# Performance work log

Hardware: AMD Instinct MI355X
Metric: run time of the kernel (lower is better)

The kernel has to match this reference:

```python
import jax, jax.numpy as jnp
import numpy as np

B, S, E, H, D, L, V, O = 64, 512, 512, 8, 64, 4, 50000, 1000
KW, STRIDE = 5, 5
L_OUT = (S - KW) // STRIDE + 1  # 102


def setup_inputs() -> dict:
    key = jax.random.key(0)
    ks = jax.random.split(key, 20)
    sc = 0.02
    inp = {
        'tokens': jax.random.randint(ks[0], (B, S), 0, V, dtype=jnp.int32),
        'emb': jax.random.normal(ks[1], (V + 1, E), jnp.float32) * sc,
        'Wq': jax.random.normal(ks[2], (L, H, E, D), jnp.float32) * sc,
        'bq': jnp.zeros((L, H, D), jnp.float32),
        'Wk': jax.random.normal(ks[3], (L, H, E, D), jnp.float32) * sc,
        'bk': jnp.zeros((L, H, D), jnp.float32),
        'Wv': jax.random.normal(ks[4], (L, H, E, D), jnp.float32) * sc,
        'bv': jnp.zeros((L, H, D), jnp.float32),
        'Wo': jax.random.normal(ks[5], (L, H * D, E), jnp.float32) * sc,
        'bo': jnp.zeros((L, E), jnp.float32),
        'W1': jax.random.normal(ks[6], (L, E, 2 * E), jnp.float32) * sc,
        'b1': jnp.zeros((L, 2 * E), jnp.float32),
        'W2': jax.random.normal(ks[7], (L, 2 * E, E), jnp.float32) * sc,
        'b2': jnp.zeros((L, E), jnp.float32),
        'Wc': jax.random.normal(ks[8], (KW, E, 1), jnp.float32) * sc,
        'bc': jnp.zeros((1,), jnp.float32),
        'Wd': jax.random.normal(ks[9], (L_OUT, O), jnp.float32) * sc,
        'bd': jnp.zeros((O,), jnp.float32),
    }
    return inp


def _l2_normalize(x, eps=1e-12):
    # tf.math.l2_normalize: x / sqrt(max(sum(x^2), eps))
    sq = jnp.sum(x * x, axis=-1, keepdims=True)
    return x * jax.lax.rsqrt(jnp.maximum(sq, eps))


def _forward(tokens, emb, Wq, bq, Wk, bk, Wv, bv, Wo, bo, W1, b1, W2, b2, Wc, bc, Wd, bd):
    mask = jnp.sign(tokens).astype(jnp.float32)[..., None]  # [B,S,1]
    out = emb[tokens] * mask                                 # [B,S,E]
    scale = 1.0 / jnp.sqrt(jnp.float32(E))                   # note: scaled by EMBEDDING_DIM, as in source
    for i in range(L):
        # per-head QKV projections, batched over heads
        q = jnp.einsum('bse,hed->bhsd', out, Wq[i]) + bq[i][None, :, None, :]
        k = jnp.einsum('bse,hed->bhsd', out, Wk[i]) + bk[i][None, :, None, :]
        v = jnp.einsum('bse,hed->bhsd', out, Wv[i]) + bv[i][None, :, None, :]
        scores = jnp.einsum('bhsd,bhtd->bhst', q, k) * scale
        attn = jax.nn.softmax(scores, axis=-1)
        heads = jnp.einsum('bhst,bhtd->bhsd', attn, v)       # [B,H,S,D]
        cat = heads.transpose(0, 2, 1, 3).reshape(B, S, H * D)
        mh = cat @ Wo[i] + bo[i]
        out = _l2_normalize(out + mh)
        ff = jax.nn.relu(out @ W1[i] + b1[i]) @ W2[i] + b2[i]
        out = ff + out
    # Conv1D(1, 5, strides=5) then squeeze channel, Dense over seq-length axis, softmax
    conv = jax.lax.conv_general_dilated(
        out, Wc, window_strides=(STRIDE,), padding='VALID',
        dimension_numbers=('NWC', 'WIO', 'NWC')) + bc          # [B,L_OUT,1]
    pooled = jnp.squeeze(conv, axis=-1)                        # [B,L_OUT]
    logits = pooled @ Wd + bd                                  # [B,O]
    return jax.nn.softmax(logits, axis=-1)


def reference(tokens, emb, Wq, bq, Wk, bk, Wv, bv, Wo, bo, W1, b1, W2, b2, Wc, bc, Wd, bd):
    return _forward(tokens, emb, Wq, bq, Wk, bk, Wv, bv, Wo, bo, W1, b1, W2, b2, Wc, bc, Wd, bd)
```

## Files before the change

### kernel.cpp

```cpp
#include <hip/hip_runtime.h>
#include <cstddef>

constexpr int B_ = 64, S_ = 512, E_ = 512, H_ = 8, D_ = 64, L_ = 4, O_ = 1000;
constexpr int BS_ = B_ * S_;
constexpr int HD_ = H_ * D_;
constexpr int QS_ = 1536;
constexpr int LOUT_ = 102;
constexpr float SCALE_ = 0.04419417382415922f;

typedef __bf16 bf16x8 __attribute__((ext_vector_type(8)));
typedef __bf16 bf16x4 __attribute__((ext_vector_type(4)));
typedef __bf16 bf16x2 __attribute__((ext_vector_type(2)));
typedef float floatx4 __attribute__((ext_vector_type(4)));

__device__ inline void load16_lds(const __bf16* g, __bf16* l) {
  __builtin_amdgcn_global_load_lds(
      (const __attribute__((address_space(1))) void*)g,
      (__attribute__((address_space(3))) void*)l, 16, 0, 0);
}

__global__ __launch_bounds__(256) void transpose_bf16(
    const float* __restrict__ in, __bf16* __restrict__ out,
    int R, int C, int IZ, int OZL, int OZH) {
  __shared__ float t[32][33];
  int z = blockIdx.z;
  const float* inz = in + (size_t)z * IZ;
  __bf16* outz = out + (size_t)(z >> 3) * OZL + (size_t)(z & 7) * OZH;
  int c0 = blockIdx.x * 32, r0 = blockIdx.y * 32;
  int x = threadIdx.x, y = threadIdx.y;
#pragma unroll
  for (int j = 0; j < 32; j += 8) t[y + j][x] = inz[(size_t)(r0 + y + j) * C + c0 + x];
  __syncthreads();
#pragma unroll
  for (int j = 0; j < 32; j += 8)
    outz[(size_t)(c0 + y + j) * R + r0 + x] = (__bf16)t[x][y + j];
}

__global__ __launch_bounds__(256) void bias_concat(
    const float* __restrict__ bq, const float* __restrict__ bk,
    const float* __restrict__ bv, float* __restrict__ qkvb) {
  int idx = blockIdx.x * 256 + threadIdx.x;
  int l = idx / QS_, j = idx % QS_;
  float v;
  if (j < 512) v = bq[l * 512 + j];
  else if (j < 1024) v = bk[l * 512 + j - 512];
  else v = bv[l * 512 + j - 1024];
  qkvb[idx] = v;
}

__global__ __launch_bounds__(256) void embed_kernel(
    const int* __restrict__ tokens, const float* __restrict__ emb,
    float* __restrict__ X, __bf16* __restrict__ Ab) {
  int idx = blockIdx.x * 256 + threadIdx.x;
  int bs = idx >> 7;
  int e = (idx & 127) << 2;
  int tok = tokens[bs];
  float4 v;
  if (tok == 0) v = make_float4(0.f, 0.f, 0.f, 0.f);
  else v = *(const float4*)(emb + (size_t)tok * E_ + e);
  size_t off = (size_t)bs * E_ + e;
  *(float4*)(X + off) = v;
  bf16x4 b;
  b[0] = (__bf16)v.x; b[1] = (__bf16)v.y; b[2] = (__bf16)v.z; b[3] = (__bf16)v.w;
  *(bf16x4*)(Ab + off) = b;
}

#define GFENCE asm volatile("" ::: "memory")
#define GBAR  do { GFENCE; __builtin_amdgcn_s_barrier(); GFENCE; } while (0)

template <int RELU, int RES, int OUTF, int OUTB, int SCQ, int KT>
__global__ __launch_bounds__(512, 2) void gemm_bf16(
    const __bf16* __restrict__ A, const __bf16* __restrict__ Bt,
    const float* __restrict__ bias, const float* __restrict__ Rsd,
    float* __restrict__ Cf, __bf16* __restrict__ Cb, int N, int lda, int Nt) {
  __shared__ __align__(16) __bf16 smem[32768];
  int tid = threadIdx.x;
  int lane = tid & 63, w8 = tid >> 6;
  int wm = w8 & 1, wn = w8 >> 1;
  int q4 = lane >> 4, a_ = lane & 15;
  int Mt8 = (int)(gridDim.x / Nt) >> 3;
  int xcd = blockIdx.x & 7;
  int j = blockIdx.x >> 3;
  int rr = j % (2 * Nt), chunk = j / (2 * Nt);
  int mt = xcd * Mt8 + chunk * 2 + (rr & 1);
  int nt = rr >> 1;
  int m0 = mt * 256, n0 = nt * 256;
  const int ldb = KT * 32;
  int ci0 = tid, ci1 = 512 + tid;
  int r0s = ci0 >> 2, q0s = (ci0 & 3) ^ ((r0s >> 1) & 3);
  int r1s = ci1 >> 2, q1s = (ci1 & 3) ^ ((r1s >> 1) & 3);
  const __bf16* Ag = A + (size_t)m0 * lda;
  const __bf16* Bg = Bt + (size_t)n0 * ldb;

  floatx4 acc[8][4];
#pragma unroll
  for (int i = 0; i < 8; ++i)
#pragma unroll
    for (int jj = 0; jj < 4; ++jj) acc[i][jj] = (floatx4)(0.0f);

  auto STAGE = [&](int t, int s) {
    __bf16* Ad = smem + s * 8192;
    __bf16* Bd = smem + 16384 + s * 8192;
    int k0 = t * 32;
    load16_lds(Ag + (size_t)r0s * lda + k0 + q0s * 8, Ad + ci0 * 8);
    load16_lds(Ag + (size_t)r1s * lda + k0 + q1s * 8, Ad + ci1 * 8);
    load16_lds(Bg + (size_t)r0s * ldb + k0 + q0s * 8, Bd + ci0 * 8);
    load16_lds(Bg + (size_t)r1s * ldb + k0 + q1s * 8, Bd + ci1 * 8);
  };

  STAGE(0, 0);
  for (int t = 0; t < KT; ++t) {
    if (t + 1 < KT) {
      STAGE(t + 1, (t + 1) & 1);
      asm volatile("s_waitcnt vmcnt(4)" ::: "memory");
    } else {
      asm volatile("s_waitcnt vmcnt(0)" ::: "memory");
    }
    GBAR;
    const __bf16* As = smem + (t & 1) * 8192;
    const __bf16* Bs = smem + 16384 + (t & 1) * 8192;
    bf16x8 bfr[4];
#pragma unroll
    for (int nf = 0; nf < 4; ++nf) {
      int r_ = wn * 64 + nf * 16 + a_;
      bfr[nf] = *(const bf16x8*)&Bs[(r_ * 4 + (q4 ^ ((r_ >> 1) & 3))) * 8];
    }
#pragma unroll
    for (int mf = 0; mf < 8; ++mf) {
      int r_ = wm * 128 + mf * 16 + a_;
      bf16x8 af = *(const bf16x8*)&As[(r_ * 4 + (q4 ^ ((r_ >> 1) & 3))) * 8];
#pragma unroll
      for (int nf = 0; nf < 4; ++nf)
        acc[mf][nf] = __builtin_amdgcn_mfma_f32_16x16x32_bf16(bfr[nf], af,
                                                              acc[mf][nf], 0, 0, 0);
    }
    GBAR;
  }

#pragma unroll 1
  for (int pass = 0; pass < 2; ++pass) {
    GBAR;
    if (wm == pass) {
#pragma unroll
      for (int mf = 0; mf < 8; ++mf) {
        int lr = mf * 16 + a_;
        int m = m0 + pass * 128 + lr;
#pragma unroll
        for (int nf = 0; nf < 4; ++nf) {
          int nl = wn * 64 + nf * 16 + q4 * 4;
          int n = n0 + nl;
          float4 bi = *(const float4*)(bias + n);
          floatx4 v = acc[mf][nf];
          v[0] += bi.x; v[1] += bi.y; v[2] += bi.z; v[3] += bi.w;
          if (SCQ) { if (n < 512) v *= SCALE_; }
          if (RES) {
            float4 rv = *(const float4*)(Rsd + (size_t)m * N + n);
            v[0] += rv.x; v[1] += rv.y; v[2] += rv.z; v[3] += rv.w;
          }
          if (RELU) {
#pragma unroll
            for (int r = 0; r < 4; ++r) v[r] = fmaxf(v[r], 0.f);
          }
          if (OUTF) {
            float4 o = make_float4(v[0], v[1], v[2], v[3]);
            *(float4*)(Cf + (size_t)m * N + n) = o;
          }
          if (OUTB) {
            bf16x4 ob;
#pragma unroll
            for (int r = 0; r < 4; ++r) ob[r] = (__bf16)v[r];
            int ch = nl >> 3;
            *(bf16x4*)&smem[lr * 256 + (ch ^ (lr & 7)) * 8 + (q4 & 1) * 4] = ob;
          }
        }
      }
    }
    GBAR;
    if (OUTB) {
#pragma unroll
      for (int it = 0; it < 8; ++it) {
        int cid = it * 512 + tid;
        int row = cid >> 5, ch = cid & 31;
        bf16x8 val = *(const bf16x8*)&smem[row * 256 + (ch ^ (row & 7)) * 8];
        *(bf16x8*)(Cb + (size_t)(m0 + pass * 128 + row) * N + n0 + ch * 8) = val;
      }
    }
  }
}

__global__ __launch_bounds__(256, 2) void attn_bf16(__bf16* __restrict__ QKV) {
  __shared__ __align__(16) __bf16 Qs[256 * 64];
  __shared__ __align__(16) __bf16 Ks[64 * 64];
  __shared__ __align__(16) __bf16 Vt[64 * 64];
  __shared__ __align__(16) __bf16 Ps[64 * 64];
  int tid = threadIdx.x, lane = tid & 63, w = tid >> 6;
  int q4 = lane >> 4, a_ = lane & 15;
  int bid = blockIdx.x;
  int xg = bid & 7, slot = bid >> 3;
  int b = (slot >> 4) * 8 + xg;
  int r_ = slot & 15;
  int h = r_ >> 1;
  int s0 = (r_ & 1) * 256;
  size_t rowbase = (size_t)b * S_ * QS_ + h * 64;
  __bf16* Qg = QKV + rowbase;
  const __bf16* Kg = QKV + rowbase + 512;
  const __bf16* Vg = QKV + rowbase + 1024;
#pragma unroll
  for (int j = 0; j < 8; ++j) {
    int ci = j * 256 + w * 64 + lane;
    int row = ci >> 3, c = ci & 7, q = c ^ (row & 7);
    load16_lds(Qg + (size_t)(s0 + row) * QS_ + q * 8, Qs + (j * 256 + w * 64) * 8);
  }
  float mrow[4], lrow[4];
  floatx4 accO[4][4];
#pragma unroll
  for (int cc = 0; cc < 4; ++cc) {
    mrow[cc] = -3.0e38f; lrow[cc] = 0.f;
#pragma unroll
    for (int jc = 0; jc < 4; ++jc) accO[cc][jc] = (floatx4)(0.0f);
  }

  for (int t0 = 0; t0 < S_; t0 += 64) {
#pragma unroll
    for (int j = 0; j < 2; ++j) {
      int ci = j * 256 + w * 64 + lane;
      int row = ci >> 3, c = ci & 7, q = c ^ (row & 7);
      load16_lds(Kg + (size_t)(t0 + row) * QS_ + q * 8, Ks + (j * 256 + w * 64) * 8);
    }
    {
      int tp = tid & 31, dg = tid >> 5;
      bf16x8 v0 = *(const bf16x8*)(Vg + (size_t)(t0 + 2 * tp) * QS_ + dg * 8);
      bf16x8 v1 = *(const bf16x8*)(Vg + (size_t)(t0 + 2 * tp + 1) * QS_ + dg * 8);
#pragma unroll
      for (int x = 0; x < 8; ++x) {
        int d = dg * 8 + x;
        bf16x2 p; p[0] = v0[x]; p[1] = v1[x];
        *(bf16x2*)&Vt[(d * 8 + ((tp >> 2) ^ (d & 7))) * 8 + (tp & 3) * 2] = p;
      }
    }
    __syncthreads();
    bf16x8 af[2][4], bv[2][4];
#pragma unroll
    for (int ks = 0; ks < 2; ++ks)
#pragma unroll
      for (int jc = 0; jc < 4; ++jc) {
        int row = jc * 16 + a_, q = ks * 4 + q4;
        af[ks][jc] = *(const bf16x8*)&Ks[(row * 8 + (q ^ (row & 7))) * 8];
        bv[ks][jc] = *(const bf16x8*)&Vt[(row * 8 + (q ^ (row & 7))) * 8];
      }
#pragma unroll
    for (int cc = 0; cc < 4; ++cc) {
      int sbase = (cc * 4 + w) * 16;
      floatx4 sc[4];
#pragma unroll
      for (int jc = 0; jc < 4; ++jc) sc[jc] = (floatx4)(0.0f);
#pragma unroll
      for (int ks = 0; ks < 2; ++ks) {
        int row = sbase + a_, q = ks * 4 + q4;
        bf16x8 bq = *(const bf16x8*)&Qs[(row * 8 + (q ^ (row & 7))) * 8];
#pragma unroll
        for (int jc = 0; jc < 4; ++jc)
          sc[jc] = __builtin_amdgcn_mfma_f32_16x16x32_bf16(af[ks][jc], bq,
                                                           sc[jc], 0, 0, 0);
      }
      float mx = sc[0][0];
#pragma unroll
      for (int jc = 0; jc < 4; ++jc)
#pragma unroll
        for (int r = 0; r < 4; ++r) mx = fmaxf(mx, sc[jc][r]);
      mx = fmaxf(mx, __shfl_xor(mx, 16));
      mx = fmaxf(mx, __shfl_xor(mx, 32));
      float mnew = fmaxf(mrow[cc], mx);
      float alpha = __expf(mrow[cc] - mnew);
      mrow[cc] = mnew;
      float ps = 0.f;
      int prow = w * 16 + a_;
#pragma unroll
      for (int jc = 0; jc < 4; ++jc) {
        bf16x4 pb;
#pragma unroll
        for (int r = 0; r < 4; ++r) {
          float p = __expf(sc[jc][r] - mnew);
          ps += p;
          pb[r] = (__bf16)p;
        }
        int pc = jc * 2 + (q4 >> 1);
        *(bf16x4*)&Ps[(prow * 8 + (pc ^ (prow & 7))) * 8 + (q4 & 1) * 4] = pb;
      }
      ps += __shfl_xor(ps, 16);
      ps += __shfl_xor(ps, 32);
      lrow[cc] = lrow[cc] * alpha + ps;
      float aal[4];
#pragma unroll
      for (int r = 0; r < 4; ++r) aal[r] = __shfl(alpha, q4 * 4 + r);
#pragma unroll
      for (int jc = 0; jc < 4; ++jc) {
        floatx4 t = accO[cc][jc];
#pragma unroll
        for (int r = 0; r < 4; ++r) t[r] *= aal[r];
        accO[cc][jc] = t;
      }
#pragma unroll
      for (int ks = 0; ks < 2; ++ks) {
        int q = ks * 4 + q4;
        bf16x8 ap = *(const bf16x8*)&Ps[(prow * 8 + (q ^ (prow & 7))) * 8];
#pragma unroll
        for (int jc = 0; jc < 4; ++jc)
          accO[cc][jc] = __builtin_amdgcn_mfma_f32_16x16x32_bf16(
              ap, bv[ks][jc], accO[cc][jc], 0, 0, 0);
      }
    }
    __syncthreads();
  }
#pragma unroll
  for (int cc = 0; cc < 4; ++cc) {
    float inv = 1.f / lrow[cc];
    float linv[4];
#pragma unroll
    for (int r = 0; r < 4; ++r) linv[r] = __shfl(inv, q4 * 4 + r);
    int srow = s0 + (cc * 4 + w) * 16 + q4 * 4;
#pragma unroll
    for (int r = 0; r < 4; ++r)
#pragma unroll
      for (int jc = 0; jc < 4; ++jc)
        Qg[(size_t)(srow + r) * QS_ + jc * 16 + a_] =
            (__bf16)(accO[cc][jc][r] * linv[r]);
  }
}

__global__ __launch_bounds__(256) void addnorm_kernel(
    float* __restrict__ X, const __bf16* __restrict__ MH, __bf16* __restrict__ Ab) {
  int row = blockIdx.x * 4 + (threadIdx.x >> 6);
  int ln = threadIdx.x & 63;
  size_t off = (size_t)row * E_ + ln * 8;
  float xv[8];
  *(float4*)&xv[0] = *(const float4*)(X + off);
  *(float4*)&xv[4] = *(const float4*)(X + off + 4);
  bf16x8 mh = *(const bf16x8*)(MH + off);
  float ss = 0.f;
#pragma unroll
  for (int j = 0; j < 8; ++j) {
    xv[j] += (float)mh[j];
    ss += xv[j] * xv[j];
  }
#pragma unroll
  for (int o = 1; o < 64; o <<= 1) ss += __shfl_xor(ss, o);
  float inv = rsqrtf(fmaxf(ss, 1e-12f));
  bf16x8 ob;
#pragma unroll
  for (int j = 0; j < 8; ++j) {
    xv[j] *= inv;
    ob[j] = (__bf16)xv[j];
  }
  *(float4*)(X + off) = *(float4*)&xv[0];
  *(float4*)(X + off + 4) = *(float4*)&xv[4];
  *(bf16x8*)(Ab + off) = ob;
}

__global__ __launch_bounds__(256) void conv_pool_kernel(
    const float* __restrict__ X, const float* __restrict__ Wc,
    const float* __restrict__ bc, float* __restrict__ pooled) {
  int wid = blockIdx.x * 4 + (threadIdx.x >> 6);
  int ln = threadIdx.x & 63;
  int b = wid / LOUT_, l = wid % LOUT_;
  const float* xr = X + (size_t)b * S_ * E_ + (size_t)l * 5 * E_;
  float v = 0.f;
#pragma unroll
  for (int j = 0; j < 10; ++j) {
    int i = (j * 64 + ln) * 4;
    float4 x4 = *(const float4*)(xr + i);
    float4 w4 = *(const float4*)(Wc + i);
    v += x4.x * w4.x + x4.y * w4.y + x4.z * w4.z + x4.w * w4.w;
  }
#pragma unroll
  for (int o = 32; o >= 1; o >>= 1) v += __shfl_down(v, o);
  if (ln == 0) pooled[b * LOUT_ + l] = v + bc[0];
}

__global__ __launch_bounds__(256) void dense_softmax_kernel(
    const float* __restrict__ pooled, const float* __restrict__ Wd,
    const float* __restrict__ bd, float* __restrict__ out) {
  __shared__ float pl[LOUT_];
  __shared__ float red[256];
  __shared__ float lg[O_];
  int b = blockIdx.x, tid = threadIdx.x;
  if (tid < LOUT_) pl[tid] = pooled[b * LOUT_ + tid];
  __syncthreads();
  for (int o = tid; o < O_; o += 256) {
    float acc = bd[o];
#pragma unroll 6
    for (int l = 0; l < LOUT_; ++l) acc += pl[l] * Wd[l * O_ + o];
    lg[o] = acc;
  }
  __syncthreads();
  float mx = -3.0e38f;
  for (int o = tid; o < O_; o += 256) mx = fmaxf(mx, lg[o]);
  red[tid] = mx;
  __syncthreads();
  for (int s2 = 128; s2 > 0; s2 >>= 1) {
    if (tid < s2) red[tid] = fmaxf(red[tid], red[tid + s2]);
    __syncthreads();
  }
  mx = red[0];
  __syncthreads();
  float se = 0.f;
  for (int o = tid; o < O_; o += 256) {
    float e = __expf(lg[o] - mx);
    lg[o] = e;
    se += e;
  }
  red[tid] = se;
  __syncthreads();
  for (int s2 = 128; s2 > 0; s2 >>= 1) {
    if (tid < s2) red[tid] += red[tid + s2];
    __syncthreads();
  }
  float inv = 1.f / red[0];
  for (int o = tid; o < O_; o += 256) out[(size_t)b * O_ + o] = lg[o] * inv;
}

extern "C" void kernel_launch(void* const* d_in, const int* in_sizes, int n_in,
                              void* d_out, int out_size, void* d_ws, size_t ws_size,
                              hipStream_t stream) {
  const int* tokens = (const int*)d_in[0];
  const float* emb = (const float*)d_in[1];
  const float* Wq = (const float*)d_in[2];
  const float* bq = (const float*)d_in[3];
  const float* Wk = (const float*)d_in[4];
  const float* bk = (const float*)d_in[5];
  const float* Wv = (const float*)d_in[6];
  const float* bv = (const float*)d_in[7];
  const float* Wo = (const float*)d_in[8];
  const float* bo = (const float*)d_in[9];
  const float* W1 = (const float*)d_in[10];
  const float* b1 = (const float*)d_in[11];
  const float* W2 = (const float*)d_in[12];
  const float* b2 = (const float*)d_in[13];
  const float* Wc = (const float*)d_in[14];
  const float* bc = (const float*)d_in[15];
  const float* Wd = (const float*)d_in[16];
  const float* bd = (const float*)d_in[17];
  float* out = (float*)d_out;

  char* ws = (char*)d_ws;
  float* X = (float*)ws;
  __bf16* Ab = (__bf16*)(ws + 67108864);
  __bf16* QKVb = (__bf16*)(ws + 100663296);
  __bf16* FF1b = QKVb;
  __bf16* MHb = (__bf16*)(ws + 201326592);
  __bf16* Wt = (__bf16*)(ws + 234881024);
  __bf16* Wt_qkv = Wt;
  __bf16* Wt_o = Wt + 3145728;
  __bf16* Wt_1 = Wt + 4194304;
  __bf16* Wt_2 = Wt + 6291456;
  float* qkvbias = (float*)(ws + 251658240);
  float* pooled = qkvbias + 6144;

  dim3 tb(32, 8);
  transpose_bf16<<<dim3(2, 16, 32), tb, 0, stream>>>(Wq, Wt_qkv + 0,      512, 64, 32768, 786432, 32768);
  transpose_bf16<<<dim3(2, 16, 32), tb, 0, stream>>>(Wk, Wt_qkv + 262144, 512, 64, 32768, 786432, 32768);
  transpose_bf16<<<dim3(2, 16, 32), tb, 0, stream>>>(Wv, Wt_qkv + 524288, 512, 64, 32768, 786432, 32768);
  transpose_bf16<<<dim3(16, 16, 4), tb, 0, stream>>>(Wo, Wt_o, 512, 512, 262144, 0, 262144);
  transpose_bf16<<<dim3(32, 16, 4), tb, 0, stream>>>(W1, Wt_1, 512, 1024, 524288, 0, 524288);
  transpose_bf16<<<dim3(16, 32, 4), tb, 0, stream>>>(W2, Wt_2, 1024, 512, 524288, 0, 524288);
  bias_concat<<<dim3(24), dim3(256), 0, stream>>>(bq, bk, bv, qkvbias);

  embed_kernel<<<dim3(BS_ * E_ / 4 / 256), dim3(256), 0, stream>>>(tokens, emb, X, Ab);

  dim3 blk(256);
  dim3 blk512(512);
  for (int i = 0; i < L_; ++i) {
    gemm_bf16<0, 0, 0, 1, 1, 16><<<dim3(768), blk512, 0, stream>>>(
        Ab, Wt_qkv + (size_t)i * 786432, qkvbias + i * QS_, nullptr, nullptr,
        QKVb, QS_, 512, 6);
    attn_bf16<<<dim3(1024), blk, 0, stream>>>(QKVb);
    gemm_bf16<0, 0, 0, 1, 0, 16><<<dim3(256), blk512, 0, stream>>>(
        QKVb, Wt_o + (size_t)i * 262144, bo + i * E_, nullptr, nullptr, MHb,
        512, QS_, 2);
    addnorm_kernel<<<dim3(BS_ / 4), blk, 0, stream>>>(X, MHb, Ab);
    gemm_bf16<1, 0, 0, 1, 0, 16><<<dim3(512), blk512, 0, stream>>>(
        Ab, Wt_1 + (size_t)i * 524288, b1 + (size_t)i * 2 * E_, nullptr, nullptr,
        FF1b, 1024, 512, 4);
    gemm_bf16<0, 1, 1, 1, 0, 32><<<dim3(256), blk512, 0, stream>>>(
        FF1b, Wt_2 + (size_t)i * 524288, b2 + (size_t)i * E_, X, X, Ab,
        512, 1024, 2);
  }
  conv_pool_kernel<<<dim3(BS_ * LOUT_ / S_ / 4), blk, 0, stream>>>(X, Wc, bc, pooled);
  dense_softmax_kernel<<<dim3(B_), blk, 0, stream>>>(pooled, Wd, bd, out);
}
```

Baseline: 1.494 ms.

## Deepen GEMM pipeline to four LDS stages with interleaved half-tile phases

Rewrites the bf16 GEMM main loop around a 4-slot LDS ring (128KB dynamic shared memory) with a K step of 64 split into halves. Each phase loads A/B fragments for half the M tile, issues the next global-to-LDS prefetch, barriers, then runs MFMAs at raised wave priority, so loads overlap with compute. KT template values are halved to match. Attention block-to-batch mapping is also changed. The larger LDS footprint may cut occupancy from the launch bound of 2 blocks per CU to 1, and the extra barriers add sync cost.

```diff
diff --git a/kernel.cpp b/kernel.cpp
--- a/kernel.cpp
+++ b/kernel.cpp
@@ -68,12 +68,56 @@
 #define GFENCE asm volatile("" ::: "memory")
 #define GBAR  do { GFENCE; __builtin_amdgcn_s_barrier(); GFENCE; } while (0)
 
+#define STAGE_A(t_, kh_)                                                       \
+  do {                                                                         \
+    __bf16* dst_ = smem + (((2 * (t_) + (kh_)) & 3) * 8192);                   \
+    load16_lds(Ag + (size_t)r0s * lda + (t_) * 64 + (kh_) * 32 + q0s * 8,      \
+               dst_ + ci0 * 8);                                                \
+    load16_lds(Ag + (size_t)r1s * lda + (t_) * 64 + (kh_) * 32 + q1s * 8,      \
+               dst_ + ci1 * 8);                                                \
+  } while (0)
+
+#define STAGE_B(t_, kh_)                                                       \
+  do {                                                                         \
+    __bf16* dst_ = smem + 32768 + (((2 * (t_) + (kh_)) & 3) * 8192);           \
+    load16_lds(Bg + (size_t)r0s * ldb + (t_) * 64 + (kh_) * 32 + q0s * 8,      \
+               dst_ + ci0 * 8);                                                \
+    load16_lds(Bg + (size_t)r1s * ldb + (t_) * 64 + (kh_) * 32 + q1s * 8,      \
+               dst_ + ci1 * 8);                                                \
+  } while (0)
+
+#define PHASE(w_, kh_, mh_, PRE)                                               \
+  do {                                                                         \
+    const __bf16* sa_ = smem + (((2 * (w_) + (kh_)) & 3) * 8192);              \
+    const __bf16* sb_ = smem + 32768 + (((2 * (w_) + (kh_)) & 3) * 8192);      \
+    bf16x8 af_[4];                                                             \
+    _Pragma("unroll") for (int mf = 0; mf < 4; ++mf) {                         \
+      int r_ = wm * 128 + ((mh_) * 4 + mf) * 16 + a_;                          \
+      af_[mf] = *(const bf16x8*)&sa_[(r_ * 4 + (q4 ^ ((r_ >> 1) & 3))) * 8];   \
+    }                                                                          \
+    if ((mh_) == 0) {                                                          \
+      _Pragma("unroll") for (int nf = 0; nf < 4; ++nf) {                       \
+        int r_ = wn * 64 + nf * 16 + a_;                                       \
+        bfc[nf] = *(const bf16x8*)&sb_[(r_ * 4 + (q4 ^ ((r_ >> 1) & 3))) * 8]; \
+      }                                                                        \
+    }                                                                          \
+    PRE;                                                                       \
+    GBAR;                                                                      \
+    __builtin_amdgcn_s_setprio(1);                                             \
+    _Pragma("unroll") for (int mf = 0; mf < 4; ++mf)                           \
+      _Pragma("unroll") for (int nf = 0; nf < 4; ++nf)                         \
+        acc[(mh_) * 4 + mf][nf] = __builtin_amdgcn_mfma_f32_16x16x32_bf16(     \
+            bfc[nf], af_[mf], acc[(mh_) * 4 + mf][nf], 0, 0, 0);               \
+    __builtin_amdgcn_s_setprio(0);                                             \
+    GBAR;                                                                      \
+  } while (0)
+
 template <int RELU, int RES, int OUTF, int OUTB, int SCQ, int KT>
 __global__ __launch_bounds__(512, 2) void gemm_bf16(
     const __bf16* __restrict__ A, const __bf16* __restrict__ Bt,
     const float* __restrict__ bias, const float* __restrict__ Rsd,
     float* __restrict__ Cf, __bf16* __restrict__ Cb, int N, int lda, int Nt) {
-  __shared__ __align__(16) __bf16 smem[32768];
+  extern __shared__ __align__(16) __bf16 smem[];
   int tid = threadIdx.x;
   int lane = tid & 63, w8 = tid >> 6;
   int wm = w8 & 1, wn = w8 >> 1;
@@ -85,7 +129,7 @@
   int mt = xcd * Mt8 + chunk * 2 + (rr & 1);
   int nt = rr >> 1;
   int m0 = mt * 256, n0 = nt * 256;
-  const int ldb = KT * 32;
+  const int ldb = KT * 64;
   int ci0 = tid, ci1 = 512 + tid;
   int r0s = ci0 >> 2, q0s = (ci0 & 3) ^ ((r0s >> 1) & 3);
   int r1s = ci1 >> 2, q1s = (ci1 & 3) ^ ((r1s >> 1) & 3);
@@ -97,45 +141,37 @@
   for (int i = 0; i < 8; ++i)
 #pragma unroll
     for (int jj = 0; jj < 4; ++jj) acc[i][jj] = (floatx4)(0.0f);
-
-  auto STAGE = [&](int t, int s) {
-    __bf16* Ad = smem + s * 8192;
-    __bf16* Bd = smem + 16384 + s * 8192;
-    int k0 = t * 32;
-    load16_lds(Ag + (size_t)r0s * lda + k0 + q0s * 8, Ad + ci0 * 8);
-    load16_lds(Ag + (size_t)r1s * lda + k0 + q1s * 8, Ad + ci1 * 8);
-    load16_lds(Bg + (size_t)r0s * ldb + k0 + q0s * 8, Bd + ci0 * 8);
-    load16_lds(Bg + (size_t)r1s * ldb + k0 + q1s * 8, Bd + ci1 * 8);
-  };
-
-  STAGE(0, 0);
-  for (int t = 0; t < KT; ++t) {
-    if (t + 1 < KT) {
-      STAGE(t + 1, (t + 1) & 1);
-      asm volatile("s_waitcnt vmcnt(4)" ::: "memory");
-    } else {
-      asm volatile("s_waitcnt vmcnt(0)" ::: "memory");
-    }
-    GBAR;
-    const __bf16* As = smem + (t & 1) * 8192;
-    const __bf16* Bs = smem + 16384 + (t & 1) * 8192;
-    bf16x8 bfr[4];
-#pragma unroll
-    for (int nf = 0; nf < 4; ++nf) {
-      int r_ = wn * 64 + nf * 16 + a_;
-      bfr[nf] = *(const bf16x8*)&Bs[(r_ * 4 + (q4 ^ ((r_ >> 1) & 3))) * 8];
-    }
-#pragma unroll
-    for (int mf = 0; mf < 8; ++mf) {
-      int r_ = wm * 128 + mf * 16 + a_;
-      bf16x8 af = *(const bf16x8*)&As[(r_ * 4 + (q4 ^ ((r_ >> 1) & 3))) * 8];
-#pragma unroll
-      for (int nf = 0; nf < 4; ++nf)
-        acc[mf][nf] = __builtin_amdgcn_mfma_f32_16x16x32_bf16(bfr[nf], af,
-                                                              acc[mf][nf], 0, 0, 0);
-    }
-    GBAR;
-  }
+  bf16x8 bfc[4];
+
+  STAGE_A(0, 0); STAGE_B(0, 0);
+  STAGE_A(0, 1); STAGE_B(0, 1);
+  STAGE_A(1, 0); STAGE_B(1, 0);
+  asm volatile("s_waitcnt vmcnt(8)" ::: "memory");
+  GBAR;
+
+  for (int w = 0; w < KT - 2; ++w) {
+    PHASE(w, 0, 0, { STAGE_A(w + 1, 1); });
+    PHASE(w, 0, 1, {
+      asm volatile("s_waitcnt vmcnt(6)" ::: "memory");
+      STAGE_B(w + 1, 1);
+    });
+    PHASE(w, 1, 0, { STAGE_A(w + 2, 0); });
+    PHASE(w, 1, 1, {
+      asm volatile("s_waitcnt vmcnt(6)" ::: "memory");
+      STAGE_B(w + 2, 0);
+    });
+  }
+  PHASE(KT - 2, 0, 0, { STAGE_A(KT - 1, 1); });
+  PHASE(KT - 2, 0, 1, {
+    asm volatile("s_waitcnt vmcnt(6)" ::: "memory");
+    STAGE_B(KT - 1, 1);
+  });
+  PHASE(KT - 2, 1, 0, {});
+  PHASE(KT - 2, 1, 1, { asm volatile("s_waitcnt vmcnt(4)" ::: "memory"); });
+  PHASE(KT - 1, 0, 0, {});
+  PHASE(KT - 1, 0, 1, { asm volatile("s_waitcnt vmcnt(0)" ::: "memory"); });
+  PHASE(KT - 1, 1, 0, {});
+  PHASE(KT - 1, 1, 1, {});
 
 #pragma unroll 1
   for (int pass = 0; pass < 2; ++pass) {
@@ -197,7 +233,7 @@
   int q4 = lane >> 4, a_ = lane & 15;
   int bid = blockIdx.x;
   int xg = bid & 7, slot = bid >> 3;
-  int b = (slot >> 4) * 8 + xg;
+  int b = xg * 8 + (slot >> 4);
   int r_ = slot & 15;
   int h = r_ >> 1;
   int s0 = (r_ & 1) * 256;
@@ -456,6 +492,16 @@
   float* qkvbias = (float*)(ws + 251658240);
   float* pooled = qkvbias + 6144;
 
+  constexpr int SMEM = 131072;
+  hipFuncSetAttribute((const void*)gemm_bf16<0, 0, 0, 1, 1, 8>,
+                      hipFuncAttributeMaxDynamicSharedMemorySize, SMEM);
+  hipFuncSetAttribute((const void*)gemm_bf16<0, 0, 0, 1, 0, 8>,
+                      hipFuncAttributeMaxDynamicSharedMemorySize, SMEM);
+  hipFuncSetAttribute((const void*)gemm_bf16<1, 0, 0, 1, 0, 8>,
+                      hipFuncAttributeMaxDynamicSharedMemorySize, SMEM);
+  hipFuncSetAttribute((const void*)gemm_bf16<0, 1, 1, 1, 0, 16>,
+                      hipFuncAttributeMaxDynamicSharedMemorySize, SMEM);
+
   dim3 tb(32, 8);
   transpose_bf16<<<dim3(2, 16, 32), tb, 0, stream>>>(Wq, Wt_qkv + 0,      512, 64, 32768, 786432, 32768);
   transpose_bf16<<<dim3(2, 16, 32), tb, 0, stream>>>(Wk, Wt_qkv + 262144, 512, 64, 32768, 786432, 32768);
@@ -470,18 +516,18 @@
   dim3 blk(256);
   dim3 blk512(512);
   for (int i = 0; i < L_; ++i) {
-    gemm_bf16<0, 0, 0, 1, 1, 16><<<dim3(768), blk512, 0, stream>>>(
+    gemm_bf16<0, 0, 0, 1, 1, 8><<<dim3(768), blk512, SMEM, stream>>>(
         Ab, Wt_qkv + (size_t)i * 786432, qkvbias + i * QS_, nullptr, nullptr,
         QKVb, QS_, 512, 6);
     attn_bf16<<<dim3(1024), blk, 0, stream>>>(QKVb);
-    gemm_bf16<0, 0, 0, 1, 0, 16><<<dim3(256), blk512, 0, stream>>>(
+    gemm_bf16<0, 0, 0, 1, 0, 8><<<dim3(256), blk512, SMEM, stream>>>(
         QKVb, Wt_o + (size_t)i * 262144, bo + i * E_, nullptr, nullptr, MHb,
         512, QS_, 2);
     addnorm_kernel<<<dim3(BS_ / 4), blk, 0, stream>>>(X, MHb, Ab);
-    gemm_bf16<1, 0, 0, 1, 0, 16><<<dim3(512), blk512, 0, stream>>>(
+    gemm_bf16<1, 0, 0, 1, 0, 8><<<dim3(512), blk512, SMEM, stream>>>(
         Ab, Wt_1 + (size_t)i * 524288, b1 + (size_t)i * 2 * E_, nullptr, nullptr,
         FF1b, 1024, 512, 4);
-    gemm_bf16<0, 1, 1, 1, 0, 32><<<dim3(256), blk512, 0, stream>>>(
+    gemm_bf16<0, 1, 1, 1, 0, 16><<<dim3(256), blk512, SMEM, stream>>>(
         FF1b, Wt_2 + (size_t)i * 524288, b2 + (size_t)i * E_, X, X, Ab,
         512, 1024, 2);
   }
```

New measurement: 1.411 ms. 1.06x faster.
